# Kernel optimization log

Hardware: AMD Instinct MI355X
Metric: run time of the kernel (lower is better)

Reference implementation:

```python
import jax, jax.numpy as jnp
import numpy as np

N_NODES = 100000
N_TRIPLES = 2000000
HIDDEN = 48


def setup_inputs() -> dict:
    key = jax.random.key(0)
    k = jax.random.split(key, 8)
    h = jax.random.normal(k[0], (N_NODES, HIDDEN), dtype=jnp.float32)
    tb_index = jax.random.randint(k[1], (N_TRIPLES, 3), 0, N_NODES, dtype=jnp.int64)
    tb_d1 = jax.random.uniform(k[2], (N_TRIPLES,), dtype=jnp.float32)
    tb_d2 = jax.random.uniform(k[3], (N_TRIPLES,), dtype=jnp.float32)
    W3 = jax.random.normal(k[4], (HIDDEN, HIDDEN), dtype=jnp.float32) / np.sqrt(HIDDEN)
    Wu = jax.random.normal(k[5], (HIDDEN, 2 * HIDDEN), dtype=jnp.float32) / np.sqrt(2 * HIDDEN)
    gamma = jnp.ones((HIDDEN,), dtype=jnp.float32)
    beta = jnp.zeros((HIDDEN,), dtype=jnp.float32)
    return {"h": h, "tb_index": tb_index, "tb_d1": tb_d1, "tb_d2": tb_d2,
            "W3": W3, "Wu": Wu, "gamma": gamma, "beta": beta}


def _layernorm(x, gamma, beta, eps=1e-5):
    mu = jnp.mean(x, axis=-1, keepdims=True)
    var = jnp.mean(jnp.square(x - mu), axis=-1, keepdims=True)
    return (x - mu) * jax.lax.rsqrt(var + eps) * gamma + beta


def reference(h, tb_index, tb_d1, tb_d2, W3, Wu, gamma, beta):
    center = tb_index[:, 0]
    nb1 = tb_index[:, 1]
    nb2 = tb_index[:, 2]
    N = h.shape[0]
    # per-triple scalar weight from distance asymmetry
    asym = jnp.abs(tb_d1 - tb_d2) / (jnp.maximum(tb_d1, tb_d2) + 1e-8)
    weight = 1.0 + 0.3 * asym                                   # [T]
    # gather -> small GEMM: msg = W_3body(h[nb1] + h[nb2])
    msg = jnp.einsum('th,oh->to', h[nb1] + h[nb2], W3)          # [T, H]
    combined = jnp.concatenate([h[center], msg], axis=-1)       # [T, 2H]
    pre = jnp.einsum('tc,oc->to', combined, Wu)                 # [T, H]
    delta = jnp.where(pre > 0, pre, 0.01 * pre) * weight[:, None]
    # scatter-add with count normalization
    nc = jax.ops.segment_sum(jnp.ones_like(weight), center, num_segments=N)
    nc = jnp.maximum(nc, 1.0)                                   # [N]
    agg = jax.ops.segment_sum(delta, center, num_segments=N)    # [N, H]
    agg = agg / jnp.sqrt(nc)[:, None]
    return _layernorm(h + agg, gamma, beta)
```

## Files before the change

kernel.cpp:

```cpp
#include <hip/hip_runtime.h>
#include <hip/hip_bf16.h>
#include <hip/hip_fp16.h>
#include <stdint.h>

#define NN 100000
#define NT 2000000
#define HD 48
#define VS 64
#define CAP 56
#define NPB 16
#define NBH ((NT + 255) / 256)
#define NB ((NN + 1023) / 1024)

#define BINB 64
#define NBIN ((NN + BINB - 1) / BINB)
#define BINCAP 1792
#define CHK 4096
#define NCHK ((NT + CHK - 1) / CHK)
#define TPT (CHK / 1024)

#define WSCALE (1.3f / 32767.0f)
#define WQUANT (32767.0f / 1.3f)

typedef _Float16 hf2 __attribute__((ext_vector_type(2)));

__device__ __forceinline__ float b2f(__hip_bfloat16 x) { return __bfloat162float(x); }

__device__ __forceinline__ float ldf(const void* p, long long i, int isbf16) {
    if (isbf16) return b2f(((const __hip_bfloat16*)p)[i]);
    return ((const float*)p)[i];
}

__device__ __forceinline__ hf2 habs2(hf2 x) {
    union { hf2 h; unsigned int u; } c; c.h = x; c.u &= 0x7FFF7FFFu; return c.h;
}
__device__ __forceinline__ hf2 splat2(float f) {
    hf2 r; r.x = (_Float16)f; r.y = (_Float16)f; return r;
}
union V4H { uint4 u; hf2 h[4]; };

__global__ __launch_bounds__(256) void prep_kernel(
        const unsigned int* __restrict__ hw, const unsigned int* __restrict__ iw,
        int* __restrict__ flags,
        const void* __restrict__ W3, const void* __restrict__ Wu,
        float* __restrict__ wu1f, float* __restrict__ bf) {
    __shared__ int cbf, cix;
    int tid = threadIdx.x;
    if (tid == 0) { cbf = 0; cix = 0; }
    __syncthreads();
    unsigned int e = (hw[tid] >> 7) & 0xff;
    if (e >= 90 && e <= 144) atomicAdd(&cbf, 1);
    if (blockIdx.x == 0 && iw[2 * tid + 1] == 0) atomicAdd(&cix, 1);
    __syncthreads();
    int fb = (cbf >= 192) ? 1 : 0;
    if (blockIdx.x == 0 && tid == 0) {
        flags[0] = fb;
        flags[1] = (cix >= 255) ? 1 : 0;
    }
    int i = blockIdx.x * 256 + tid;
    if (i < HD * HD) {
        int o = i / HD, hh = i % HD;
        wu1f[i] = ldf(Wu, o * 2 * HD + hh, fb);
        float s = 0.f;
        #pragma unroll 8
        for (int k = 0; k < HD; ++k)
            s += ldf(Wu, o * 2 * HD + HD + k, fb) * ldf(W3, k * HD + hh, fb);
        bf[i] = s;
    }
}

__global__ __launch_bounds__(256) void node_kernel(
        const void* __restrict__ h, const int* __restrict__ flags,
        const float* __restrict__ wu1f, const float* __restrict__ bf,
        __half* __restrict__ uh, __half* __restrict__ vh) {
    __shared__ float Ws[HD * 49];
    __shared__ float Bs[HD * 49];
    __shared__ float hs[NPB * HD];
    int tid = threadIdx.x;
    int fb = flags[0];
    for (int i = tid; i < HD * HD; i += 256) {
        int o = i / HD, hh = i % HD;
        Ws[o * 49 + hh] = wu1f[i];
        Bs[o * 49 + hh] = bf[i];
    }
    int base = blockIdx.x * NPB;
    for (int i = tid; i < NPB * HD; i += 256)
        hs[i] = ldf(h, (long long)base * HD + i, fb);
    {
        int ln = tid >> 4, o = HD + (tid & 15);
        vh[(size_t)(base + ln) * VS + o] = (__half)0.f;
    }
    __syncthreads();
    for (int i = tid; i < NPB * HD; i += 256) {
        int ln = i / HD, o = i - ln * HD;
        const float* hr = hs + ln * HD;
        const float* wr = Ws + o * 49;
        const float* br = Bs + o * 49;
        float su = 0.f, sv = 0.f;
        #pragma unroll
        for (int k = 0; k < HD; ++k) { float hv = hr[k]; su += wr[k] * hv; sv += br[k] * hv; }
        int n = base + ln;
        uh[(size_t)n * HD + o] = __float2half(su);
        vh[(size_t)n * VS + o] = __float2half(sv);
    }
}

__global__ __launch_bounds__(1024) void binA_kernel(
        const void* __restrict__ idxp,
        const void* __restrict__ d1p, const void* __restrict__ d2p,
        const int* __restrict__ flags, int* __restrict__ gcur,
        uint2* __restrict__ binned) {
    __shared__ int h1[NBIN];
    __shared__ int h2[NBIN];
    __shared__ int gb[NBIN];
    int tid = threadIdx.x;
    for (int i = tid; i < NBIN; i += 1024) { h1[i] = 0; h2[i] = 0; }
    __syncthreads();
    int t0 = blockIdx.x * CHK;
    int fb = flags[0], fi = flags[1];
    const int* qi = (const int*)idxp;

    unsigned mx[TPT], my[TPT];
    int bn[TPT];
    #pragma unroll
    for (int j = 0; j < TPT; ++j) {
        int t = t0 + j * 1024 + tid;
        if (t < NT) {
            int c, n1, n2;
            if (fi) {
                c  = qi[6LL * t];
                n1 = qi[6LL * t + 2];
                n2 = qi[6LL * t + 4];
            } else {
                c  = qi[3LL * t];
                n1 = qi[3LL * t + 1];
                n2 = qi[3LL * t + 2];
            }
            float d1 = ldf(d1p, t, fb);
            float d2 = ldf(d2p, t, fb);
            float asym = fabsf(d1 - d2) / (fmaxf(d1, d2) + 1e-8f);
            unsigned qw = (unsigned)((1.0f + 0.3f * asym) * WQUANT + 0.5f);
            if (qw > 32767u) qw = 32767u;
            bn[j] = c >> 6;
            mx[j] = (unsigned)n1 | (qw << 17);
            my[j] = (unsigned)n2 | ((unsigned)(c & 63) << 17);
            atomicAdd(&h1[bn[j]], 1);
        } else {
            bn[j] = -1;
        }
    }
    __syncthreads();
    for (int b = tid; b < NBIN; b += 1024) {
        int n = h1[b];
        gb[b] = n ? atomicAdd(&gcur[b << 5], n) : 0;
    }
    __syncthreads();
    #pragma unroll
    for (int j = 0; j < TPT; ++j) {
        if (bn[j] >= 0) {
            int r = atomicAdd(&h2[bn[j]], 1);
            int pos = gb[bn[j]] + r;
            if (pos < BINCAP)
                binned[(size_t)bn[j] * BINCAP + pos] = make_uint2(mx[j], my[j]);
        }
    }
}

__global__ __launch_bounds__(512, 4) void bin_accum_kernel(
        const void* __restrict__ h, const int* __restrict__ flags,
        const __half* __restrict__ uh, const __half* __restrict__ vh,
        const int* __restrict__ gcur, const uint2* __restrict__ binned,
        const void* __restrict__ gamma, const void* __restrict__ beta,
        void* __restrict__ out) {
    __shared__ uint2 buckets[BINB][64];
    __shared__ int   cur[BINB];
    __shared__ float ucs[8][64];
    __shared__ float accs[8][HD];
    int tid = threadIdx.x, fb = flags[0];
    int bin = blockIdx.x;

    for (int i = tid; i < BINB; i += 512) cur[i] = 0;
    __syncthreads();

    int nm = gcur[bin << 5]; if (nm > BINCAP) nm = BINCAP;
    const uint2* bp = binned + (size_t)bin * BINCAP;
    for (int i = tid; i < nm; i += 512) {
        uint2 m = bp[i];
        int cl = (m.y >> 17) & (BINB - 1);
        int r = atomicAdd(&cur[cl], 1);
        if (r < CAP) buckets[cl][r] = m;
    }
    __syncthreads();

    int wv = tid >> 6, lane = tid & 63;
    int s = lane >> 3, dg = lane & 7;
    const char* vb = (const char*)vh;
    size_t dgo = (size_t)dg * 16;
    float gv = (lane < HD) ? ldf(gamma, lane, fb) : 0.f;
    float bv = (lane < HD) ? ldf(beta, lane, fb) : 0.f;

    for (int ci = 0; ci < BINB / 8; ++ci) {
        int cl = wv * (BINB / 8) + ci;
        int n = bin * BINB + cl;
        if (n >= NN) continue;

        int m = cur[cl]; if (m > CAP) m = CAP;
        float hval = (lane < HD) ? ldf(h, (long long)n * HD + lane, fb) : 0.f;
        float uval = (lane < HD) ? __half2float(uh[(size_t)n * HD + lane]) : 0.f;
        ucs[wv][lane] = uval;
        hf2 uc4[4];
        #pragma unroll
        for (int j = 0; j < 4; ++j) {
            uc4[j].x = (_Float16)ucs[wv][dg * 8 + 2 * j];
            uc4[j].y = (_Float16)ucs[wv][dg * 8 + 2 * j + 1];
        }

        float accf[8] = {0.f, 0.f, 0.f, 0.f, 0.f, 0.f, 0.f, 0.f};
        for (int t = 0; t < m; t += 16) {
            uint2 m0 = buckets[cl][t + s];
            uint2 m1 = buckets[cl][t + 8 + s];
            int v0 = (t + s) < m, v1 = (t + 8 + s) < m;
            unsigned a0 = v0 ? (m0.x & 0x1FFFFu) : 0u;
            unsigned b0 = v0 ? (m0.y & 0x1FFFFu) : 0u;
            float w0 = v0 ? (float)(m0.x >> 17) * WSCALE : 0.f;
            unsigned a1 = v1 ? (m1.x & 0x1FFFFu) : 0u;
            unsigned b1 = v1 ? (m1.y & 0x1FFFFu) : 0u;
            float w1 = v1 ? (float)(m1.x >> 17) * WSCALE : 0.f;
            V4H pa0, pb0, pa1, pb1;
            pa0.u = *(const uint4*)(vb + (size_t)a0 * 128 + dgo);
            pb0.u = *(const uint4*)(vb + (size_t)b0 * 128 + dgo);
            pa1.u = *(const uint4*)(vb + (size_t)a1 * 128 + dgo);
            pb1.u = *(const uint4*)(vb + (size_t)b1 * 128 + dgo);
            hf2 aw0 = splat2(0.505f * w0), bw0 = splat2(0.495f * w0);
            hf2 aw1 = splat2(0.505f * w1), bw1 = splat2(0.495f * w1);
            #pragma unroll
            for (int j = 0; j < 4; ++j) {
                hf2 p0 = pa0.h[j] + pb0.h[j] + uc4[j];
                hf2 acch = p0 * aw0 + habs2(p0) * bw0;
                hf2 p1 = pa1.h[j] + pb1.h[j] + uc4[j];
                acch += p1 * aw1 + habs2(p1) * bw1;
                accf[2 * j]     += (float)acch.x;
                accf[2 * j + 1] += (float)acch.y;
            }
        }

        #pragma unroll
        for (int j = 0; j < 8; ++j) {
            accf[j] += __shfl_xor(accf[j], 8, 64);
            accf[j] += __shfl_xor(accf[j], 16, 64);
            accf[j] += __shfl_xor(accf[j], 32, 64);
        }
        if (lane < 6) {
            #pragma unroll
            for (int j = 0; j < 8; ++j) accs[wv][lane * 8 + j] = accf[j];
        }
        float av = (lane < HD) ? accs[wv][lane] : 0.f;

        float rnc = rsqrtf(fmaxf((float)m, 1.0f));
        float x = (lane < HD) ? (hval + av * rnc) : 0.f;
        float su = x, sq = x * x;
        #pragma unroll
        for (int o = 32; o; o >>= 1) {
            su += __shfl_xor(su, o, 64);
            sq += __shfl_xor(sq, o, 64);
        }
        float mu   = su * (1.0f / HD);
        float var  = sq * (1.0f / HD) - mu * mu;
        float rstd = rsqrtf(var + 1e-5f);
        if (lane < HD) {
            float r = (x - mu) * rstd * gv + bv;
            if (fb) ((__hip_bfloat16*)out)[(size_t)n * HD + lane] = __float2bfloat16(r);
            else    ((float*)out)[(size_t)n * HD + lane] = r;
        }
    }
}

__global__ __launch_bounds__(256) void hist_kernel(const void* __restrict__ idxp,
                                                   const int* __restrict__ flags,
                                                   int* __restrict__ cnt) {
    int t = blockIdx.x * 256 + threadIdx.x;
    if (t >= NT) return;
    int c = flags[1] ? (int)((const long long*)idxp)[3LL * t]
                     : ((const int*)idxp)[3 * t];
    atomicAdd(&cnt[c << 4], 1);
}

__global__ __launch_bounds__(1024) void scan_part(const int* __restrict__ cnt,
                                                  int* __restrict__ off,
                                                  int* __restrict__ bsum) {
    __shared__ int wsums[16];
    int tid = threadIdx.x, lane = tid & 63, wv = tid >> 6;
    int i = blockIdx.x * 1024 + tid;
    int x = (i < NN) ? cnt[i << 4] : 0;
    int vx = x;
    #pragma unroll
    for (int o = 1; o < 64; o <<= 1) {
        int y = __shfl_up(vx, o, 64);
        if (lane >= o) vx += y;
    }
    if (lane == 63) wsums[wv] = vx;
    __syncthreads();
    if (tid == 0) {
        int s = 0;
        #pragma unroll
        for (int k = 0; k < 16; ++k) { int t2 = wsums[k]; wsums[k] = s; s += t2; }
        bsum[blockIdx.x] = s;
    }
    __syncthreads();
    if (i < NN) off[i] = wsums[wv] + vx - x;
}

__global__ __launch_bounds__(1024) void scan_add(int* __restrict__ off,
                                                 const int* __restrict__ bsum) {
    int bid = blockIdx.x;
    int pre = 0;
    for (int k = 0; k < bid; ++k) pre += bsum[k];
    int i = bid * 1024 + threadIdx.x;
    if (i < NN) off[i] += pre;
}

__global__ __launch_bounds__(256) void scatter_kernel(
        const void* __restrict__ idxp,
        const void* __restrict__ d1p, const void* __restrict__ d2p,
        const int* __restrict__ flags, int* __restrict__ cur,
        uint2* __restrict__ sp) {
    int t = blockIdx.x * 256 + threadIdx.x;
    if (t >= NT) return;
    int fb = flags[0];
    int c, n1, n2;
    if (flags[1]) {
        const long long* q = (const long long*)idxp;
        c = (int)q[3LL * t]; n1 = (int)q[3LL * t + 1]; n2 = (int)q[3LL * t + 2];
    } else {
        const int* q = (const int*)idxp;
        c = q[3 * t]; n1 = q[3 * t + 1]; n2 = q[3 * t + 2];
    }
    float d1 = ldf(d1p, t, fb);
    float d2 = ldf(d2p, t, fb);
    float asym = fabsf(d1 - d2) / (fmaxf(d1, d2) + 1e-8f);
    unsigned int qw = (unsigned int)((1.0f + 0.3f * asym) * WQUANT + 0.5f);
    if (qw > 32767u) qw = 32767u;
    uint2 m = make_uint2((unsigned int)n1 | (qw << 17), (unsigned int)n2);
    int pos = atomicAdd(&cur[c], 1);
    sp[pos] = m;
}

__global__ __launch_bounds__(256) void accum_kernel(
        const void* __restrict__ h, const int* __restrict__ flags,
        const __half* __restrict__ uh, const __half* __restrict__ vh,
        const int* __restrict__ seg, const uint2* __restrict__ sp,
        const void* __restrict__ gamma, const void* __restrict__ beta,
        void* __restrict__ out) {
    __shared__ uint2 metas[4][64];
    __shared__ float ucs[4][64];
    __shared__ float accs[4][HD];
    int tid = threadIdx.x, fb = flags[0];
    int wv = tid >> 6, lane = tid & 63;
    int n = blockIdx.x * 4 + wv;

    float hval = (lane < HD) ? ldf(h, (long long)n * HD + lane, fb) : 0.f;
    float uval = (lane < HD) ? __half2float(uh[(size_t)n * HD + lane]) : 0.f;
    ucs[wv][lane] = uval;

    int s = lane >> 3, dg = lane & 7;
    hf2 uc4[4];
    #pragma unroll
    for (int j = 0; j < 4; ++j) {
        uc4[j].x = (_Float16)ucs[wv][dg * 8 + 2 * j];
        uc4[j].y = (_Float16)ucs[wv][dg * 8 + 2 * j + 1];
    }

    int start = (n == 0) ? 0 : seg[n - 1];
    int end = seg[n];
    float accf[8] = {0.f, 0.f, 0.f, 0.f, 0.f, 0.f, 0.f, 0.f};
    const char* vb = (const char*)vh;
    size_t dgo = (size_t)dg * 16;

    for (int chunk = start; chunk < end; chunk += 64) {
        int m = end - chunk; if (m > 64) m = 64;
        if (lane < m) metas[wv][lane] = sp[chunk + lane];
        for (int t = 0; t < m; t += 16) {
            uint2 m0 = metas[wv][t + s];
            uint2 m1 = metas[wv][t + 8 + s];
            int v0 = (t + s) < m, v1 = (t + 8 + s) < m;
            unsigned a0 = v0 ? (m0.x & 0x1FFFFu) : 0u;
            unsigned b0 = v0 ? (m0.y & 0x1FFFFu) : 0u;
            float w0 = v0 ? (float)(m0.x >> 17) * WSCALE : 0.f;
            unsigned a1 = v1 ? (m1.x & 0x1FFFFu) : 0u;
            unsigned b1 = v1 ? (m1.y & 0x1FFFFu) : 0u;
            float w1 = v1 ? (float)(m1.x >> 17) * WSCALE : 0.f;
            V4H pa0, pb0, pa1, pb1;
            pa0.u = *(const uint4*)(vb + (size_t)a0 * 128 + dgo);
            pb0.u = *(const uint4*)(vb + (size_t)b0 * 128 + dgo);
            pa1.u = *(const uint4*)(vb + (size_t)a1 * 128 + dgo);
            pb1.u = *(const uint4*)(vb + (size_t)b1 * 128 + dgo);
            hf2 aw0 = splat2(0.505f * w0), bw0 = splat2(0.495f * w0);
            hf2 aw1 = splat2(0.505f * w1), bw1 = splat2(0.495f * w1);
            #pragma unroll
            for (int j = 0; j < 4; ++j) {
                hf2 p0 = pa0.h[j] + pb0.h[j] + uc4[j];
                hf2 acch = p0 * aw0 + habs2(p0) * bw0;
                hf2 p1 = pa1.h[j] + pb1.h[j] + uc4[j];
                acch += p1 * aw1 + habs2(p1) * bw1;
                accf[2 * j]     += (float)acch.x;
                accf[2 * j + 1] += (float)acch.y;
            }
        }
    }

    #pragma unroll
    for (int j = 0; j < 8; ++j) {
        accf[j] += __shfl_xor(accf[j], 8, 64);
        accf[j] += __shfl_xor(accf[j], 16, 64);
        accf[j] += __shfl_xor(accf[j], 32, 64);
    }
    if (lane < 6) {
        #pragma unroll
        for (int j = 0; j < 8; ++j) accs[wv][lane * 8 + j] = accf[j];
    }
    float av = (lane < HD) ? accs[wv][lane] : 0.f;

    float rnc = rsqrtf(fmaxf((float)(end - start), 1.0f));
    float x = (lane < HD) ? (hval + av * rnc) : 0.f;
    float su = x, sq = x * x;
    #pragma unroll
    for (int o = 32; o; o >>= 1) {
        su += __shfl_xor(su, o, 64);
        sq += __shfl_xor(sq, o, 64);
    }
    float mu   = su * (1.0f / HD);
    float var  = sq * (1.0f / HD) - mu * mu;
    float rstd = rsqrtf(var + 1e-5f);
    if (lane < HD) {
        float g  = ldf(gamma, lane, fb);
        float bb = ldf(beta, lane, fb);
        float r = (x - mu) * rstd * g + bb;
        if (fb) ((__hip_bfloat16*)out)[(size_t)n * HD + lane] = __float2bfloat16(r);
        else    ((float*)out)[(size_t)n * HD + lane] = r;
    }
}

extern "C" void kernel_launch(void* const* d_in, const int* in_sizes, int n_in,
                              void* d_out, int out_size, void* d_ws, size_t ws_size,
                              hipStream_t stream) {
    const void* h     = d_in[0];
    const void* idx   = d_in[1];
    const void* d1    = d_in[2];
    const void* d2    = d_in[3];
    const void* W3    = d_in[4];
    const void* Wu    = d_in[5];
    const void* gamma = d_in[6];
    const void* beta  = d_in[7];

    char* base  = (char*)d_ws;
    int*   flags = (int*)base;
    float* wu1f  = (float*)(base + 64);
    float* bf    = wu1f + HD * HD;
    uintptr_t ua = (uintptr_t)(bf + HD * HD);
    __half* uh   = (__half*)((ua + 127) & ~(uintptr_t)127);
    __half* vh   = (__half*)((char*)uh + (size_t)NN * HD * 2);
    char*  after = (char*)vh + (size_t)NN * VS * 2;

    int*   gcur = (int*)after;
    uintptr_t bna = (uintptr_t)(gcur + (size_t)NBIN * 32);
    uint2* binned = (uint2*)((bna + 127) & ~(uintptr_t)127);
    size_t need_primary = ((char*)(binned + (size_t)NBIN * BINCAP)) - base;

    int*   cnt  = (int*)after;
    int*   off  = (int*)(cnt + (size_t)NN * 16);
    int*   bsum = off + NN;
    uintptr_t spa = (uintptr_t)(bsum + 256);
    uint2* sp   = (uint2*)((spa + 15) & ~(uintptr_t)15);

    prep_kernel<<<(HD * HD + 255) / 256, 256, 0, stream>>>(
        (const unsigned int*)h, (const unsigned int*)idx, flags, W3, Wu, wu1f, bf);
    node_kernel<<<NN / NPB, 256, 0, stream>>>(h, flags, wu1f, bf, uh, vh);

    if (ws_size >= need_primary) {
        hipMemsetAsync(gcur, 0, (size_t)NBIN * 32 * sizeof(int), stream);
        binA_kernel<<<NCHK, 1024, 0, stream>>>(idx, d1, d2, flags, gcur, binned);
        bin_accum_kernel<<<NBIN, 512, 0, stream>>>(h, flags, uh, vh, gcur, binned,
                                                   gamma, beta, d_out);
    } else {
        hipMemsetAsync(cnt, 0, (size_t)NN * 16 * sizeof(int), stream);
        hist_kernel<<<NBH, 256, 0, stream>>>(idx, flags, cnt);
        scan_part<<<NB, 1024, 0, stream>>>(cnt, off, bsum);
        scan_add<<<NB, 1024, 0, stream>>>(off, bsum);
        scatter_kernel<<<(NT + 255) / 256, 256, 0, stream>>>(
            idx, d1, d2, flags, off, sp);
        accum_kernel<<<NN / 4, 256, 0, stream>>>(h, flags, uh, vh, off, sp,
                                                 gamma, beta, d_out);
    }
}
```

Measured before the change: 275.5 us.

## Fuse node projection and triple binning into one launch, zero counters in prep

Merges the per-node projection kernel and the triple-binning kernel into a single launch. Block ranges pick the role, and the two roles share shared memory through a union. The separate memset of the bin cursors is dropped; prep_kernel now clears them. Triples per binning chunk double and nodes per node block go from 16 to 20. The aim is to cut launch and memset overhead and let node and binning work overlap on the GPU, at the cost of 1024-thread node blocks that are mostly idle and tighter register limits on the binning path.

```diff
diff --git a/kernel.cpp b/kernel.cpp
--- a/kernel.cpp
+++ b/kernel.cpp
@@ -8,16 +8,18 @@
 #define HD 48
 #define VS 64
 #define CAP 56
-#define NPB 16
+#define NPB 20
 #define NBH ((NT + 255) / 256)
 #define NB ((NN + 1023) / 1024)
 
 #define BINB 64
 #define NBIN ((NN + BINB - 1) / BINB)
 #define BINCAP 1792
-#define CHK 4096
+#define CHK 8192
 #define NCHK ((NT + CHK - 1) / CHK)
 #define TPT (CHK / 1024)
+#define NNODEB (NN / NPB)
+#define FATGRID (NCHK + NNODEB)
 
 #define WSCALE (1.3f / 32767.0f)
 #define WQUANT (32767.0f / 1.3f)
@@ -43,7 +45,8 @@
         const unsigned int* __restrict__ hw, const unsigned int* __restrict__ iw,
         int* __restrict__ flags,
         const void* __restrict__ W3, const void* __restrict__ Wu,
-        float* __restrict__ wu1f, float* __restrict__ bf) {
+        float* __restrict__ wu1f, float* __restrict__ bf,
+        int* __restrict__ gcur) {
     __shared__ int cbf, cix;
     int tid = threadIdx.x;
     if (tid == 0) { cbf = 0; cix = 0; }
@@ -57,6 +60,8 @@
         flags[0] = fb;
         flags[1] = (cix >= 255) ? 1 : 0;
     }
+    for (int i = blockIdx.x * 256 + tid; i < NBIN * 32; i += 9 * 256)
+        gcur[i] = 0;
     int i = blockIdx.x * 256 + tid;
     if (i < HD * HD) {
         int o = i / HD, hh = i % HD;
@@ -69,99 +74,97 @@
     }
 }
 
-__global__ __launch_bounds__(256) void node_kernel(
+struct NodeLds { float Ws[HD * 49]; float Bs[HD * 49]; float hs[NPB * HD]; };
+struct BinLds  { int h1[NBIN]; int h2[NBIN]; int gb[NBIN]; };
+union FatLds   { NodeLds n; BinLds b; };
+
+__global__ __launch_bounds__(1024, 2) void fused_nb_kernel(
         const void* __restrict__ h, const int* __restrict__ flags,
         const float* __restrict__ wu1f, const float* __restrict__ bf,
-        __half* __restrict__ uh, __half* __restrict__ vh) {
-    __shared__ float Ws[HD * 49];
-    __shared__ float Bs[HD * 49];
-    __shared__ float hs[NPB * HD];
+        __half* __restrict__ uh, __half* __restrict__ vh,
+        const void* __restrict__ idxp,
+        const void* __restrict__ d1p, const void* __restrict__ d2p,
+        int* __restrict__ gcur, uint2* __restrict__ binned) {
+    __shared__ FatLds L;
     int tid = threadIdx.x;
     int fb = flags[0];
-    for (int i = tid; i < HD * HD; i += 256) {
-        int o = i / HD, hh = i % HD;
-        Ws[o * 49 + hh] = wu1f[i];
-        Bs[o * 49 + hh] = bf[i];
-    }
-    int base = blockIdx.x * NPB;
-    for (int i = tid; i < NPB * HD; i += 256)
-        hs[i] = ldf(h, (long long)base * HD + i, fb);
-    {
-        int ln = tid >> 4, o = HD + (tid & 15);
-        vh[(size_t)(base + ln) * VS + o] = (__half)0.f;
-    }
-    __syncthreads();
-    for (int i = tid; i < NPB * HD; i += 256) {
-        int ln = i / HD, o = i - ln * HD;
-        const float* hr = hs + ln * HD;
-        const float* wr = Ws + o * 49;
-        const float* br = Bs + o * 49;
-        float su = 0.f, sv = 0.f;
-        #pragma unroll
-        for (int k = 0; k < HD; ++k) { float hv = hr[k]; su += wr[k] * hv; sv += br[k] * hv; }
-        int n = base + ln;
-        uh[(size_t)n * HD + o] = __float2half(su);
-        vh[(size_t)n * VS + o] = __float2half(sv);
-    }
-}
-
-__global__ __launch_bounds__(1024) void binA_kernel(
-        const void* __restrict__ idxp,
-        const void* __restrict__ d1p, const void* __restrict__ d2p,
-        const int* __restrict__ flags, int* __restrict__ gcur,
-        uint2* __restrict__ binned) {
-    __shared__ int h1[NBIN];
-    __shared__ int h2[NBIN];
-    __shared__ int gb[NBIN];
-    int tid = threadIdx.x;
-    for (int i = tid; i < NBIN; i += 1024) { h1[i] = 0; h2[i] = 0; }
-    __syncthreads();
-    int t0 = blockIdx.x * CHK;
-    int fb = flags[0], fi = flags[1];
-    const int* qi = (const int*)idxp;
-
-    unsigned mx[TPT], my[TPT];
-    int bn[TPT];
-    #pragma unroll
-    for (int j = 0; j < TPT; ++j) {
-        int t = t0 + j * 1024 + tid;
-        if (t < NT) {
-            int c, n1, n2;
-            if (fi) {
-                c  = qi[6LL * t];
-                n1 = qi[6LL * t + 2];
-                n2 = qi[6LL * t + 4];
+
+    if (blockIdx.x < NCHK) {
+        int fi = flags[1];
+        for (int i = tid; i < NBIN; i += 1024) { L.b.h1[i] = 0; L.b.h2[i] = 0; }
+        __syncthreads();
+        int t0 = blockIdx.x * CHK;
+        const int* qi = (const int*)idxp;
+
+        unsigned mx[TPT], my[TPT];
+        int bn[TPT];
+        #pragma unroll
+        for (int j = 0; j < TPT; ++j) {
+            int t = t0 + j * 1024 + tid;
+            if (t < NT) {
+                int c, n1, n2;
+                if (fi) {
+                    c  = qi[6LL * t];
+                    n1 = qi[6LL * t + 2];
+                    n2 = qi[6LL * t + 4];
+                } else {
+                    c  = qi[3LL * t];
+                    n1 = qi[3LL * t + 1];
+                    n2 = qi[3LL * t + 2];
+                }
+                float d1 = ldf(d1p, t, fb);
+                float d2 = ldf(d2p, t, fb);
+                float asym = fabsf(d1 - d2) / (fmaxf(d1, d2) + 1e-8f);
+                unsigned qw = (unsigned)((1.0f + 0.3f * asym) * WQUANT + 0.5f);
+                if (qw > 32767u) qw = 32767u;
+                bn[j] = c >> 6;
+                mx[j] = (unsigned)n1 | (qw << 17);
+                my[j] = (unsigned)n2 | ((unsigned)(c & 63) << 17);
+                atomicAdd(&L.b.h1[bn[j]], 1);
             } else {
-                c  = qi[3LL * t];
-                n1 = qi[3LL * t + 1];
-                n2 = qi[3LL * t + 2];
+                bn[j] = -1;
             }
-            float d1 = ldf(d1p, t, fb);
-            float d2 = ldf(d2p, t, fb);
-            float asym = fabsf(d1 - d2) / (fmaxf(d1, d2) + 1e-8f);
-            unsigned qw = (unsigned)((1.0f + 0.3f * asym) * WQUANT + 0.5f);
-            if (qw > 32767u) qw = 32767u;
-            bn[j] = c >> 6;
-            mx[j] = (unsigned)n1 | (qw << 17);
-            my[j] = (unsigned)n2 | ((unsigned)(c & 63) << 17);
-            atomicAdd(&h1[bn[j]], 1);
-        } else {
-            bn[j] = -1;
-        }
-    }
-    __syncthreads();
-    for (int b = tid; b < NBIN; b += 1024) {
-        int n = h1[b];
-        gb[b] = n ? atomicAdd(&gcur[b << 5], n) : 0;
-    }
-    __syncthreads();
-    #pragma unroll
-    for (int j = 0; j < TPT; ++j) {
-        if (bn[j] >= 0) {
-            int r = atomicAdd(&h2[bn[j]], 1);
-            int pos = gb[bn[j]] + r;
-            if (pos < BINCAP)
-                binned[(size_t)bn[j] * BINCAP + pos] = make_uint2(mx[j], my[j]);
+        }
+        __syncthreads();
+        for (int b = tid; b < NBIN; b += 1024) {
+            int n = L.b.h1[b];
+            L.b.gb[b] = n ? atomicAdd(&gcur[b << 5], n) : 0;
+        }
+        __syncthreads();
+        #pragma unroll
+        for (int j = 0; j < TPT; ++j) {
+            if (bn[j] >= 0) {
+                int r = atomicAdd(&L.b.h2[bn[j]], 1);
+                int pos = L.b.gb[bn[j]] + r;
+                if (pos < BINCAP)
+                    binned[(size_t)bn[j] * BINCAP + pos] = make_uint2(mx[j], my[j]);
+            }
+        }
+    } else {
+        int base = (blockIdx.x - NCHK) * NPB;
+        for (int i = tid; i < HD * HD; i += 1024) {
+            int o = i / HD, hh = i % HD;
+            L.n.Ws[o * 49 + hh] = wu1f[i];
+            L.n.Bs[o * 49 + hh] = bf[i];
+        }
+        for (int i = tid; i < NPB * HD; i += 1024)
+            L.n.hs[i] = ldf(h, (long long)base * HD + i, fb);
+        if (tid < NPB * 16) {
+            int ln = tid >> 4, o = HD + (tid & 15);
+            vh[(size_t)(base + ln) * VS + o] = (__half)0.f;
+        }
+        __syncthreads();
+        for (int i = tid; i < NPB * HD; i += 1024) {
+            int ln = i / HD, o = i - ln * HD;
+            const float* hr = L.n.hs + ln * HD;
+            const float* wr = L.n.Ws + o * 49;
+            const float* br = L.n.Bs + o * 49;
+            float su = 0.f, sv = 0.f;
+            #pragma unroll
+            for (int k = 0; k < HD; ++k) { float hv = hr[k]; su += wr[k] * hv; sv += br[k] * hv; }
+            int n = base + ln;
+            uh[(size_t)n * HD + o] = __float2half(su);
+            vh[(size_t)n * VS + o] = __float2half(sv);
         }
     }
 }
@@ -272,6 +275,42 @@
             if (fb) ((__hip_bfloat16*)out)[(size_t)n * HD + lane] = __float2bfloat16(r);
             else    ((float*)out)[(size_t)n * HD + lane] = r;
         }
+    }
+}
+
+__global__ __launch_bounds__(256) void node_kernel(
+        const void* __restrict__ h, const int* __restrict__ flags,
+        const float* __restrict__ wu1f, const float* __restrict__ bf,
+        __half* __restrict__ uh, __half* __restrict__ vh) {
+    __shared__ float Ws[HD * 49];
+    __shared__ float Bs[HD * 49];
+    __shared__ float hs[16 * HD];
+    int tid = threadIdx.x;
+    int fb = flags[0];
+    for (int i = tid; i < HD * HD; i += 256) {
+        int o = i / HD, hh = i % HD;
+        Ws[o * 49 + hh] = wu1f[i];
+        Bs[o * 49 + hh] = bf[i];
+    }
+    int base = blockIdx.x * 16;
+    for (int i = tid; i < 16 * HD; i += 256)
+        hs[i] = ldf(h, (long long)base * HD + i, fb);
+    {
+        int ln = tid >> 4, o = HD + (tid & 15);
+        vh[(size_t)(base + ln) * VS + o] = (__half)0.f;
+    }
+    __syncthreads();
+    for (int i = tid; i < 16 * HD; i += 256) {
+        int ln = i / HD, o = i - ln * HD;
+        const float* hr = hs + ln * HD;
+        const float* wr = Ws + o * 49;
+        const float* br = Bs + o * 49;
+        float su = 0.f, sv = 0.f;
+        #pragma unroll
+        for (int k = 0; k < HD; ++k) { float hv = hr[k]; su += wr[k] * hv; sv += br[k] * hv; }
+        int n = base + ln;
+        uh[(size_t)n * HD + o] = __float2half(su);
+        vh[(size_t)n * VS + o] = __float2half(sv);
     }
 }
 
@@ -473,15 +512,16 @@
     uint2* sp   = (uint2*)((spa + 15) & ~(uintptr_t)15);
 
     prep_kernel<<<(HD * HD + 255) / 256, 256, 0, stream>>>(
-        (const unsigned int*)h, (const unsigned int*)idx, flags, W3, Wu, wu1f, bf);
-    node_kernel<<<NN / NPB, 256, 0, stream>>>(h, flags, wu1f, bf, uh, vh);
+        (const unsigned int*)h, (const unsigned int*)idx, flags, W3, Wu,
+        wu1f, bf, gcur);
 
     if (ws_size >= need_primary) {
-        hipMemsetAsync(gcur, 0, (size_t)NBIN * 32 * sizeof(int), stream);
-        binA_kernel<<<NCHK, 1024, 0, stream>>>(idx, d1, d2, flags, gcur, binned);
+        fused_nb_kernel<<<FATGRID, 1024, 0, stream>>>(
+            h, flags, wu1f, bf, uh, vh, idx, d1, d2, gcur, binned);
         bin_accum_kernel<<<NBIN, 512, 0, stream>>>(h, flags, uh, vh, gcur, binned,
                                                    gamma, beta, d_out);
     } else {
+        node_kernel<<<NN / 16, 256, 0, stream>>>(h, flags, wu1f, bf, uh, vh);
         hipMemsetAsync(cnt, 0, (size_t)NN * 16 * sizeof(int), stream);
         hist_kernel<<<NBH, 256, 0, stream>>>(idx, flags, cnt);
         scan_part<<<NB, 1024, 0, stream>>>(cnt, off, bsum);
```

Measured after the change: 261.1 us. -5.2%, faster.
